# Kernel optimization log

Hardware: AMD Instinct MI355X
Metric: run time of the kernel (lower is better)

## Reference

```python
import jax, jax.numpy as jnp
import numpy as np

# dims
B, N, D = 256, 77, 768     # batch, CLIP tokens, token dim
K, Dn, H = 16, 768, 8      # nodes, node dim, heads
HID, L = 512, 2            # edge-MLP hidden, num GNN layers


def setup_inputs() -> dict:
    key = jax.random.key(0)
    ks = jax.random.split(key, 12)
    g = lambda k, shape, s=0.02: (jax.random.normal(k, shape, jnp.float32) * s)
    return {
        "w": jax.random.normal(ks[0], (B, N, D), jnp.float32),
        "token_mask": jax.random.randint(ks[1], (B, N), 0, 2).astype(jnp.int32),
        "node_queries": g(ks[2], (1, K, Dn)),
        "Wq": g(ks[3], (Dn, Dn)), "bq": jnp.zeros((Dn,), jnp.float32),
        "Wk": g(ks[4], (D, Dn)),  "bk": jnp.zeros((Dn,), jnp.float32),
        "Wv": g(ks[5], (D, Dn)),  "bv": jnp.zeros((Dn,), jnp.float32),
        "We1": g(ks[6], (2 * Dn, HID)), "be1": jnp.zeros((HID,), jnp.float32),
        "We2": g(ks[7], (HID, 1)),      "be2": jnp.zeros((1,), jnp.float32),
        "fuse_gate": jnp.float32(0.0),
        "Wg": g(ks[8], (L, Dn, Dn)), "bg": jnp.zeros((L, Dn), jnp.float32),
    }


def _edge_logits(V, We1, be1, We2, be2):
    # edge_mlp(cat[Vi, Vj]) without materializing [B,K,K,2Dn]:
    # split first linear into the Vi-half and Vj-half of its weight.
    hi = V @ We1[:Dn]   # [B,K,HID]
    hj = V @ We1[Dn:]   # [B,K,HID]
    h = jax.nn.relu(hi[:, :, None, :] + hj[:, None, :, :] + be1)  # [B,K,K,HID]
    return jnp.einsum('bijh,h->bij', h, We2[:, 0]) + be2[0]       # [B,K,K]


def _forward(w, node_queries, Wq, bq, Wk, bk, Wv, bv,
             We1, be1, We2, be2, fuse_gate, Wg, bg, token_mask):
    q = jnp.broadcast_to(node_queries, (B, K, Dn))
    Q = q @ Wq + bq        # [B,K,Dn]
    Kt = w @ Wk + bk       # [B,N,Dn]
    Vt = w @ Wv + bv       # [B,N,Dn]
    # per-head dot products summed over heads == full Dn dot product
    scale = (Dn // H) ** -0.5
    scores = jnp.einsum('bkd,bnd->bkn', Q, Kt) * scale  # [B,K,N]
    pad = (token_mask == 0)[:, None, :]                 # [B,1,N]
    scores = jnp.where(pad, jnp.finfo(scores.dtype).min, scores)
    # softmax over K per token (transpose to [B,N,K])
    S = jax.nn.softmax(jnp.swapaxes(scores, 1, 2), axis=-1)  # [B,N,K]
    V = jnp.einsum('bnk,bnd->bkd', S, Vt)                    # [B,K,Dn]
    gate = jax.nn.sigmoid(fuse_gate)
    V = (1.0 - gate) * V + gate * q
    # pre-GNN edge logits, then relational GNN refinement
    E = _edge_logits(V, We1, be1, We2, be2)
    A = jax.nn.softmax(E, axis=-1)  # [B,K,K], fixed across layers
    for l in range(L):
        msg = jnp.einsum('bij,bjd->bid', A, V @ Wg[l] + bg[l])
        V = V + jax.nn.relu(msg)
    # post-GNN edge logits
    E = _edge_logits(V, We1, be1, We2, be2)
    return S, V, E


def reference(w, token_mask, node_queries, Wq, bq, Wk, bk, Wv, bv,
              We1, be1, We2, be2, fuse_gate, Wg, bg):
    return _forward(w, node_queries, Wq, bq, Wk, bk, Wv, bv,
                    We1, be1, We2, be2, fuse_gate, Wg, bg, token_mask)
```

## Files before the change

kernel.cpp:

```cpp
#include <hip/hip_runtime.h>

typedef unsigned short u16;
typedef __attribute__((ext_vector_type(8))) short short8;
typedef __attribute__((ext_vector_type(4))) float f32x4;

#define DEV static __device__ __forceinline__

DEV float bf2f(u16 u) { return __uint_as_float(((unsigned)u) << 16); }
DEV u16 f2bf(float f) {
  unsigned u = __float_as_uint(f);
  return (u16)((u + 0x7fffu + ((u >> 16) & 1u)) >> 16);
}

DEV void cp16(void* lds, const void* g) {
  __builtin_amdgcn_global_load_lds(
      (const __attribute__((address_space(1))) unsigned int*)g,
      (__attribute__((address_space(3))) unsigned int*)lds, 16, 0, 0);
}


__global__ __launch_bounds__(256) void wcast_k(const float* __restrict__ src,
                                               u16* __restrict__ dst, int n8) {
  int i = blockIdx.x * 256 + threadIdx.x;
  if (i >= n8) return;
  f32x4 a = *(const f32x4*)&src[(size_t)i * 8];
  f32x4 b = *(const f32x4*)&src[(size_t)i * 8 + 4];
  short8 o;
#pragma unroll
  for (int e = 0; e < 4; ++e) { o[e] = (short)f2bf(a[e]); o[e + 4] = (short)f2bf(b[e]); }
  *(short8*)&dst[(size_t)i * 8] = o;
}

__global__ __launch_bounds__(256) void tcast_all(const float* __restrict__ Wv,
                                                 const float* __restrict__ We1,
                                                 const float* __restrict__ Wg,
                                                 u16* __restrict__ WvT,
                                                 u16* __restrict__ We1T,
                                                 u16* __restrict__ WgT) {
  __shared__ float tile[32][33];
  const float* src; u16* dst; int C;
  switch (blockIdx.z) {
    case 0: src = Wv;           dst = WvT;           C = 768; break;
    case 1: src = We1;          dst = We1T;          C = 512; break;
    case 2: src = We1 + 393216; dst = We1T + 393216; C = 512; break;
    case 3: src = Wg;           dst = WgT;           C = 768; break;
    default: src = Wg + 589824; dst = WgT + 589824;  C = 768; break;
  }
  int r0 = blockIdx.y * 32, c0 = blockIdx.x * 32;
  if (c0 >= C) return;
  int tr = threadIdx.x >> 5, tc = threadIdx.x & 31;
#pragma unroll
  for (int rr = 0; rr < 4; ++rr)
    tile[tr + rr * 8][tc] = src[(size_t)(r0 + tr + rr * 8) * C + c0 + tc];
  __syncthreads();
#pragma unroll
  for (int rr = 0; rr < 4; ++rr)
    dst[(size_t)(c0 + tr + rr * 8) * 768 + r0 + tc] = f2bf(tile[tc][tr + rr * 8]);
}

__global__ __launch_bounds__(256) void q_part(const float* __restrict__ nq,
                                              const float* __restrict__ Wq,
                                              float* __restrict__ Qpart) {
  int gid = blockIdx.x * 256 + threadIdx.x;
  int s = blockIdx.y;
  int k = gid / 768, d = gid % 768;
  const float* nr = nq + k * 768 + s * 96;
  const float* wp = Wq + (size_t)(s * 96) * 768 + d;
  float s0 = 0.f, s1 = 0.f, s2 = 0.f, s3 = 0.f;
#pragma unroll
  for (int c = 0; c < 96; c += 4) {
    s0 += nr[c + 0] * wp[(size_t)(c + 0) * 768];
    s1 += nr[c + 1] * wp[(size_t)(c + 1) * 768];
    s2 += nr[c + 2] * wp[(size_t)(c + 2) * 768];
    s3 += nr[c + 3] * wp[(size_t)(c + 3) * 768];
  }
  Qpart[(size_t)s * 12288 + gid] = (s0 + s1) + (s2 + s3);
}

__global__ __launch_bounds__(256) void q_reduce(const float* __restrict__ Qpart,
                                                const float* __restrict__ bq,
                                                float* __restrict__ Qf) {
  int gid = blockIdx.x * 256 + threadIdx.x;
  int d = gid % 768;
  float s = bq[d];
#pragma unroll
  for (int i = 0; i < 8; ++i) s += Qpart[(size_t)i * 12288 + gid];
  Qf[gid] = s;
}

__global__ __launch_bounds__(256) void pt_kernel(const float* __restrict__ Qf,
                                                 const float* __restrict__ Wk,
                                                 const float* __restrict__ bk,
                                                 u16* __restrict__ PT16,
                                                 float* __restrict__ qb) {
  int t = threadIdx.x;
  if (blockIdx.x == 48) {
    int k = t >> 4, j = t & 15;
    const float* q = Qf + k * 768 + j * 48;
    const float* bp = bk + j * 48;
    float s = 0.f;
#pragma unroll
    for (int d = 0; d < 48; d += 4) {
      f32x4 qv = *(const f32x4*)&q[d];
      f32x4 bv4 = *(const f32x4*)&bp[d];
      s += qv[0] * bv4[0] + qv[1] * bv4[1] + qv[2] * bv4[2] + qv[3] * bv4[3];
    }
#pragma unroll
    for (int off = 1; off < 16; off <<= 1) s += __shfl_xor(s, off);
    if (j == 0) qb[k] = s;
    return;
  }
  int gid = blockIdx.x * 256 + t;
  int c = gid >> 4, k = gid & 15;
  const float* wr = Wk + (size_t)c * 768;
  const float* q = Qf + k * 768;
  float s = 0.f;
  for (int d = 0; d < 768; d += 4) {
    f32x4 wv = *(const f32x4*)&wr[d];
    f32x4 qv = *(const f32x4*)&q[d];
    s += wv[0] * qv[0] + wv[1] * qv[1] + wv[2] * qv[2] + wv[3] * qv[3];
  }
  PT16[k * 768 + c] = f2bf(s);
}

__global__ __launch_bounds__(256) void score2(const u16* __restrict__ w16,
                                              const u16* __restrict__ PT16,
                                              const float* __restrict__ qb,
                                              const int* __restrict__ mask,
                                              float* __restrict__ Sout) {
  __shared__ u16 Ps[16 * 776];
  int t = threadIdx.x, wave = t >> 6, lane = t & 63, l16 = lane & 15, quad = lane >> 4;
  int m0 = blockIdx.x * 64;
#pragma unroll
  for (int r = 0; r < 6; ++r) {
    int idx = t + 256 * r;
    int row = idx / 96, c8 = idx % 96;
    *(short8*)&Ps[row * 776 + c8 * 8] = *(const short8*)&PT16[row * 768 + c8 * 8];
  }
  __syncthreads();
  int row = m0 + wave * 16 + l16;
  const u16* ap = w16 + (size_t)row * 768 + quad * 8;
  f32x4 acc = {0.f, 0.f, 0.f, 0.f};
#pragma unroll
  for (int it = 0; it < 24; ++it) {
    short8 fa = *(const short8*)(ap + it * 32);
    short8 fb = *(const short8*)&Ps[l16 * 776 + it * 32 + quad * 8];
    acc = __builtin_amdgcn_mfma_f32_16x16x32_bf16(fa, fb, acc, 0, 0, 0);
  }
  float qv = qb[l16];
  const float scale = 0.1020620726159658f;
#pragma unroll
  for (int r = 0; r < 4; ++r) {
    int orow = m0 + wave * 16 + quad * 4 + r;
    float s = (acc[r] + qv) * scale;
    if (mask[orow] == 0) s = -3.402823466e38f;
    float mx = s;
#pragma unroll
    for (int off = 1; off < 16; off <<= 1) mx = fmaxf(mx, __shfl_xor(mx, off));
    float e = __expf(s - mx);
    float sm = e;
#pragma unroll
    for (int off = 1; off < 16; off <<= 1) sm += __shfl_xor(sm, off);
    Sout[(size_t)orow * 16 + l16] = e / sm;
  }
}

__global__ __launch_bounds__(256) void u_kernel(const float* __restrict__ Sg,
                                                const u16* __restrict__ w16,
                                                u16* __restrict__ U16,
                                                float* __restrict__ sk) {
  __shared__ float Ss[1232];
  int b = blockIdx.x, t = threadIdx.x;
  int d = blockIdx.y * 256 + t;
#pragma unroll
  for (int r = 0; r < 5; ++r) {
    int idx = t + 256 * r;
    if (idx < 1232) Ss[idx] = Sg[(size_t)b * 1232 + idx];
  }
  __syncthreads();
  float a[16];
#pragma unroll
  for (int k = 0; k < 16; ++k) a[k] = 0.f;
  const u16* wp = w16 + (size_t)b * 59136;
  for (int n = 0; n < 77; ++n) {
    float g = bf2f(wp[(size_t)n * 768 + d]);
    const float* sr = &Ss[n * 16];
#pragma unroll
    for (int k = 0; k < 16; ++k) a[k] += sr[k] * g;
  }
#pragma unroll
  for (int k = 0; k < 16; ++k)
    U16[(size_t)b * 12288 + (size_t)k * 768 + d] = f2bf(a[k]);
  if (blockIdx.y == 0 && t < 16) {
    float s = 0.f;
    for (int n = 0; n < 77; ++n) s += Ss[n * 16 + t];
    sk[b * 16 + t] = s;
  }
}

__global__ __launch_bounds__(256) void vgemm(const u16* __restrict__ A,
                                             const u16* __restrict__ BT,
                                             const float* __restrict__ skp,
                                             const float* __restrict__ bv,
                                             const float* __restrict__ nq,
                                             const float* __restrict__ gatep,
                                             float* __restrict__ V32,
                                             u16* __restrict__ V16) {
  __shared__ u16 As[64 * 32];
  __shared__ u16 Bs[128 * 32];
  int mi = blockIdx.x / 6, ni = blockIdx.x % 6;
  int m0 = mi * 64, n0 = ni * 128;
  int t = threadIdx.x;
  int wave = t >> 6, lane = t & 63, l16 = lane & 15, quad = lane >> 4;
  int ra = wave * 16 + (lane >> 2);
  int rb1 = wave * 32 + (lane >> 2);
  int rb2 = rb1 + 16;
  int cslot = lane & 3;
  int cga = (cslot ^ ((ra >> 1) & 3)) * 8;
  int cgb1 = (cslot ^ ((rb1 >> 1) & 3)) * 8;
  int cgb2 = (cslot ^ ((rb2 >> 1) & 3)) * 8;

  f32x4 zero4 = {0.f, 0.f, 0.f, 0.f};
  f32x4 acc[4][2];
#pragma unroll
  for (int i = 0; i < 4; ++i) { acc[i][0] = zero4; acc[i][1] = zero4; }

  for (int k0 = 0; k0 < 768; k0 += 32) {
    cp16(&As[(wave * 16) * 32],      A + (size_t)(m0 + ra) * 768 + k0 + cga);
    cp16(&Bs[(wave * 32) * 32],      BT + (size_t)(n0 + rb1) * 768 + k0 + cgb1);
    cp16(&Bs[(wave * 32 + 16) * 32], BT + (size_t)(n0 + rb2) * 768 + k0 + cgb2);
    __syncthreads();
    short8 fa[4], fb[2];
#pragma unroll
    for (int i = 0; i < 4; ++i) {
      int R = i * 16 + l16;
      fa[i] = *(const short8*)&As[R * 32 + (quad ^ ((R >> 1) & 3)) * 8];
    }
#pragma unroll
    for (int j = 0; j < 2; ++j) {
      int R = wave * 32 + j * 16 + l16;
      fb[j] = *(const short8*)&Bs[R * 32 + (quad ^ ((R >> 1) & 3)) * 8];
    }
#pragma unroll
    for (int i = 0; i < 4; ++i)
#pragma unroll
      for (int j = 0; j < 2; ++j)
        acc[i][j] = __builtin_amdgcn_mfma_f32_16x16x32_bf16(fa[i], fb[j], acc[i][j], 0, 0, 0);
    __syncthreads();
  }

  float gv = gatep[0];
  float g = 1.f / (1.f + __expf(-gv)), og = 1.f - g;
  int narr[2]; float bvj[2];
#pragma unroll
  for (int j = 0; j < 2; ++j) {
    narr[j] = n0 + wave * 32 + j * 16 + l16;
    bvj[j] = bv[narr[j]];
  }
#pragma unroll
  for (int i = 0; i < 4; ++i)
#pragma unroll
    for (int r = 0; r < 4; ++r) {
      int m = m0 + i * 16 + quad * 4 + r;
      float skv = skp[m];
      size_t mrow = (size_t)m * 768;
      const float* nqr = nq + (m & 15) * 768;
#pragma unroll
      for (int j = 0; j < 2; ++j) {
        float val = acc[i][j][r] + skv * bvj[j];
        float v = og * val + g * nqr[narr[j]];
        V32[mrow + narr[j]] = v;
        V16[mrow + narr[j]] = f2bf(v);
      }
    }
}

__global__ __launch_bounds__(256) void gemm16s(const u16* __restrict__ A,
                                               const u16* __restrict__ BT0,
                                               const float* __restrict__ bias0,
                                               u16* __restrict__ C0, int N0, int ntA,
                                               const u16* __restrict__ BT1,
                                               const float* __restrict__ bias1,
                                               u16* __restrict__ C1, int N1, int ntB,
                                               int K) {
  __shared__ u16 As[64 * 32];
  __shared__ u16 Bs[128 * 32];
  int nt = ntA + ntB;
  int mi = blockIdx.x / nt, ni = blockIdx.x % nt;
  const u16* BT; const float* bias; u16* C; int N, n0;
  if (ni < ntA) { BT = BT0; bias = bias0; C = C0; N = N0; n0 = ni * 128; }
  else          { BT = BT1; bias = bias1; C = C1; N = N1; n0 = (ni - ntA) * 128; }
  int m0 = mi * 64;
  int t = threadIdx.x;
  int wave = t >> 6, lane = t & 63, l16 = lane & 15, quad = lane >> 4;
  int ra = wave * 16 + (lane >> 2);
  int rb1 = wave * 32 + (lane >> 2);
  int rb2 = rb1 + 16;
  int cslot = lane & 3;
  int cga = (cslot ^ ((ra >> 1) & 3)) * 8;
  int cgb1 = (cslot ^ ((rb1 >> 1) & 3)) * 8;
  int cgb2 = (cslot ^ ((rb2 >> 1) & 3)) * 8;

  f32x4 zero4 = {0.f, 0.f, 0.f, 0.f};
  f32x4 acc[4][2];
#pragma unroll
  for (int i = 0; i < 4; ++i) { acc[i][0] = zero4; acc[i][1] = zero4; }

  for (int k0 = 0; k0 < K; k0 += 32) {
    cp16(&As[(wave * 16) * 32],      A + (size_t)(m0 + ra) * K + k0 + cga);
    cp16(&Bs[(wave * 32) * 32],      BT + (size_t)(n0 + rb1) * K + k0 + cgb1);
    cp16(&Bs[(wave * 32 + 16) * 32], BT + (size_t)(n0 + rb2) * K + k0 + cgb2);
    __syncthreads();
    short8 fa[4], fb[2];
#pragma unroll
    for (int i = 0; i < 4; ++i) {
      int R = i * 16 + l16;
      fa[i] = *(const short8*)&As[R * 32 + (quad ^ ((R >> 1) & 3)) * 8];
    }
#pragma unroll
    for (int j = 0; j < 2; ++j) {
      int R = wave * 32 + j * 16 + l16;
      fb[j] = *(const short8*)&Bs[R * 32 + (quad ^ ((R >> 1) & 3)) * 8];
    }
#pragma unroll
    for (int i = 0; i < 4; ++i)
#pragma unroll
      for (int j = 0; j < 2; ++j)
        acc[i][j] = __builtin_amdgcn_mfma_f32_16x16x32_bf16(fa[i], fb[j], acc[i][j], 0, 0, 0);
    __syncthreads();
  }

  int narr[2]; float bvj[2];
#pragma unroll
  for (int j = 0; j < 2; ++j) {
    narr[j] = n0 + wave * 32 + j * 16 + l16;
    bvj[j] = bias ? bias[narr[j]] : 0.f;
  }
#pragma unroll
  for (int i = 0; i < 4; ++i)
#pragma unroll
    for (int r = 0; r < 4; ++r) {
      size_t mrow = (size_t)(m0 + i * 16 + quad * 4 + r) * N;
#pragma unroll
      for (int j = 0; j < 2; ++j)
        C[mrow + narr[j]] = f2bf(acc[i][j][r] + bvj[j]);
    }
}

__global__ __launch_bounds__(256) void edge_kernel(const u16* __restrict__ HIJ,
                                                   const float* __restrict__ be1,
                                                   const float* __restrict__ We2,
                                                   const float* __restrict__ be2v,
                                                   float* __restrict__ Aout,
                                                   float* __restrict__ Eout) {
  __shared__ float hiS[16 * 260];
  __shared__ float hjS[16 * 260];
  __shared__ float be1s[512];
  __shared__ float w2s[512];
  int b = blockIdx.x, t = threadIdx.x;
  be1s[t] = be1[t]; be1s[t + 256] = be1[t + 256];
  w2s[t] = We2[t];  w2s[t + 256] = We2[t + 256];

  int i = t >> 4, jj = t & 15;
  float e = 0.f;
  for (int half = 0; half < 2; ++half) {
    __syncthreads();
#pragma unroll
    for (int r = 0; r < 2; ++r) {
      int idx = t + 256 * r;
      int row = idx >> 5, c8 = idx & 31;
      const u16* src = &HIJ[(size_t)(b * 16 + row) * 1024 + half * 256 + c8 * 8];
      short8 hv = *(const short8*)src;
      short8 jv = *(const short8*)(src + 512);
      f32x4 l0, l1, m0v, m1v;
#pragma unroll
      for (int ee = 0; ee < 4; ++ee) {
        l0[ee] = bf2f((u16)hv[ee]); l1[ee] = bf2f((u16)hv[ee + 4]);
        m0v[ee] = bf2f((u16)jv[ee]); m1v[ee] = bf2f((u16)jv[ee + 4]);
      }
      *(f32x4*)&hiS[row * 260 + c8 * 8] = l0;
      *(f32x4*)&hiS[row * 260 + c8 * 8 + 4] = l1;
      *(f32x4*)&hjS[row * 260 + c8 * 8] = m0v;
      *(f32x4*)&hjS[row * 260 + c8 * 8 + 4] = m1v;
    }
    __syncthreads();
    const float* hi = &hiS[i * 260];
    const float* hj = &hjS[jj * 260];
    const float* b1 = &be1s[half * 256];
    const float* w2 = &w2s[half * 256];
#pragma unroll 2
    for (int h4 = 0; h4 < 64; ++h4) {
      f32x4 hv = *(const f32x4*)&hi[h4 * 4];
      f32x4 jv = *(const f32x4*)&hj[h4 * 4];
      f32x4 bv = *(const f32x4*)&b1[h4 * 4];
      f32x4 wv = *(const f32x4*)&w2[h4 * 4];
#pragma unroll
      for (int ee = 0; ee < 4; ++ee)
        e += fmaxf(hv[ee] + jv[ee] + bv[ee], 0.f) * wv[ee];
    }
  }
  e += be2v[0];

  if (Aout) {
    float mx = e;
#pragma unroll
    for (int off = 1; off < 16; off <<= 1) mx = fmaxf(mx, __shfl_xor(mx, off));
    float ex = __expf(e - mx);
    float sm = ex;
#pragma unroll
    for (int off = 1; off < 16; off <<= 1) sm += __shfl_xor(sm, off);
    Aout[(size_t)b * 256 + t] = ex / sm;
  }
  if (Eout) Eout[(size_t)b * 256 + t] = e;
}

__global__ __launch_bounds__(256) void combine_kernel(const float* __restrict__ Aws,
                                                      const u16* __restrict__ G,
                                                      float* __restrict__ V32,
                                                      u16* __restrict__ V16,
                                                      float* __restrict__ Vout) {
  __shared__ float Gs[16 * 772];
  __shared__ float As[256];
  int b = blockIdx.x, t = threadIdx.x;
#pragma unroll
  for (int r = 0; r < 6; ++r) {
    int idx = t + 256 * r;
    int row = idx / 96, c8 = idx % 96;
    short8 gv8 = *(const short8*)&G[(size_t)(b * 16 + row) * 768 + c8 * 8];
    f32x4 l0, l1;
#pragma unroll
    for (int ee = 0; ee < 4; ++ee) { l0[ee] = bf2f((u16)gv8[ee]); l1[ee] = bf2f((u16)gv8[ee + 4]); }
    *(f32x4*)&Gs[row * 772 + c8 * 8] = l0;
    *(f32x4*)&Gs[row * 772 + c8 * 8 + 4] = l1;
  }
  As[t] = Aws[(size_t)b * 256 + t];
  __syncthreads();
#pragma unroll
  for (int m = 0; m < 3; ++m) {
    int d = t + m * 256;
    float gv[16];
#pragma unroll
    for (int j = 0; j < 16; ++j) gv[j] = Gs[j * 772 + d];
#pragma unroll
    for (int i = 0; i < 16; ++i) {
      float msg = 0.f;
#pragma unroll
      for (int j = 0; j < 16; ++j) msg += As[i * 16 + j] * gv[j];
      size_t idx = (size_t)b * 12288 + (size_t)i * 768 + d;
      float v = V32[idx] + fmaxf(msg, 0.f);
      V32[idx] = v;
      V16[idx] = f2bf(v);
      if (Vout) Vout[idx] = v;
    }
  }
}

extern "C" void kernel_launch(void* const* d_in, const int* in_sizes, int n_in,
                              void* d_out, int out_size, void* d_ws, size_t ws_size,
                              hipStream_t stream) {
  const float* w    = (const float*)d_in[0];
  const int*   mask = (const int*)d_in[1];
  const float* nq   = (const float*)d_in[2];
  const float* Wq   = (const float*)d_in[3];
  const float* bq   = (const float*)d_in[4];
  const float* Wk   = (const float*)d_in[5];
  const float* bk   = (const float*)d_in[6];
  const float* Wv   = (const float*)d_in[7];
  const float* bv   = (const float*)d_in[8];
  const float* We1  = (const float*)d_in[9];
  const float* be1  = (const float*)d_in[10];
  const float* We2  = (const float*)d_in[11];
  const float* be2  = (const float*)d_in[12];
  const float* gate = (const float*)d_in[13];
  const float* Wg   = (const float*)d_in[14];
  const float* bg   = (const float*)d_in[15];

  float* ws    = (float*)d_ws;
  float* V32   = ws;
  float* Aws   = V32 + 3145728;
  float* Qpart = Aws + 65536;
  float* Qf    = Qpart + 98304;
  float* qb    = Qf + 12288;
  float* sk    = qb + 16;
  u16* PT16    = (u16*)(sk + 4096);
  u16* WvT     = PT16 + 12288;
  u16* We1T    = WvT + 589824;
  u16* WgT     = We1T + 786432;
  u16* V16     = WgT + 1179648;
  u16* U16     = V16 + 3145728;
  u16* w16     = U16 + 3145728;
  u16* HIJ     = w16;
  u16* Gws     = w16 + 4194304;

  float* out  = (float*)d_out;
  float* Sout = out;
  float* Vout = out + 315392;
  float* Eout = out + 315392 + 3145728;

  dim3 blk(256);

  tcast_all<<<dim3(24, 24, 5), blk, 0, stream>>>(Wv, We1, Wg, WvT, We1T, WgT);
  wcast_k<<<7392, blk, 0, stream>>>(w, w16, 1892352);
  q_part<<<dim3(48, 8), blk, 0, stream>>>(nq, Wq, Qpart);
  q_reduce<<<48, blk, 0, stream>>>(Qpart, bq, Qf);
  pt_kernel<<<49, blk, 0, stream>>>(Qf, Wk, bk, PT16, qb);

  score2<<<308, blk, 0, stream>>>(w16, PT16, qb, mask, Sout);

  u_kernel<<<dim3(256, 3), blk, 0, stream>>>(Sout, w16, U16, sk);
  vgemm<<<384, blk, 0, stream>>>(U16, WvT, sk, bv, nq, gate, V32, V16);

  gemm16s<<<896, blk, 0, stream>>>(V16, We1T, nullptr, HIJ, 1024, 8,
                                   WgT, bg, Gws, 768, 6, 768);
  edge_kernel<<<256, blk, 0, stream>>>(HIJ, be1, We2, be2, Aws, (float*)nullptr);
  combine_kernel<<<256, blk, 0, stream>>>(Aws, Gws, V32, V16, (float*)nullptr);

  gemm16s<<<384, blk, 0, stream>>>(V16, WgT + 589824, bg + 768, Gws, 768, 6,
                                   WgT + 589824, bg + 768, Gws, 768, 0, 768);
  combine_kernel<<<256, blk, 0, stream>>>(Aws, Gws, V32, V16, Vout);

  gemm16s<<<512, blk, 0, stream>>>(V16, We1T, nullptr, HIJ, 1024, 8,
                                   We1T, nullptr, HIJ, 1024, 0, 768);
  edge_kernel<<<256, blk, 0, stream>>>(HIJ, be1, We2, be2, (float*)nullptr, Eout);
}
```

Measured before the change: 344.9 us.

## Drop w bf16 cast pass and double-buffer LDS in GEMM kernels

Removes the separate wcast_k kernel that converted w to bf16. score2 now converts fp32 w inline, and u_kernel reads fp32 w directly. This saves a full write and reread of a roughly 60 MB tensor, at the cost of those kernels reading fp32, which is twice the bytes of bf16. Separately, vgemm and gemm16s now double-buffer their LDS tiles so the next k-tile's global-to-LDS copy overlaps the current MFMA work, using an explicit vmcnt drain plus barrier instead of two syncthreads per iteration.

New measurement: 330.4 us. 1.04x faster.

```diff
diff --git a/kernel.cpp b/kernel.cpp
--- a/kernel.cpp
+++ b/kernel.cpp
@@ -18,18 +18,8 @@
       (__attribute__((address_space(3))) unsigned int*)lds, 16, 0, 0);
 }
 
-
-__global__ __launch_bounds__(256) void wcast_k(const float* __restrict__ src,
-                                               u16* __restrict__ dst, int n8) {
-  int i = blockIdx.x * 256 + threadIdx.x;
-  if (i >= n8) return;
-  f32x4 a = *(const f32x4*)&src[(size_t)i * 8];
-  f32x4 b = *(const f32x4*)&src[(size_t)i * 8 + 4];
-  short8 o;
-#pragma unroll
-  for (int e = 0; e < 4; ++e) { o[e] = (short)f2bf(a[e]); o[e + 4] = (short)f2bf(b[e]); }
-  *(short8*)&dst[(size_t)i * 8] = o;
-}
+DEV void vm_drain() { asm volatile("s_waitcnt vmcnt(0)" ::: "memory"); }
+
 
 __global__ __launch_bounds__(256) void tcast_all(const float* __restrict__ Wv,
                                                  const float* __restrict__ We1,
@@ -123,7 +113,7 @@
   PT16[k * 768 + c] = f2bf(s);
 }
 
-__global__ __launch_bounds__(256) void score2(const u16* __restrict__ w16,
+__global__ __launch_bounds__(256) void score2(const float* __restrict__ w,
                                               const u16* __restrict__ PT16,
                                               const float* __restrict__ qb,
                                               const int* __restrict__ mask,
@@ -139,11 +129,15 @@
   }
   __syncthreads();
   int row = m0 + wave * 16 + l16;
-  const u16* ap = w16 + (size_t)row * 768 + quad * 8;
+  const float* ap = w + (size_t)row * 768 + quad * 8;
   f32x4 acc = {0.f, 0.f, 0.f, 0.f};
 #pragma unroll
   for (int it = 0; it < 24; ++it) {
-    short8 fa = *(const short8*)(ap + it * 32);
+    f32x4 a0 = *(const f32x4*)(ap + it * 32);
+    f32x4 a1 = *(const f32x4*)(ap + it * 32 + 4);
+    short8 fa;
+#pragma unroll
+    for (int e = 0; e < 4; ++e) { fa[e] = (short)f2bf(a0[e]); fa[e + 4] = (short)f2bf(a1[e]); }
     short8 fb = *(const short8*)&Ps[l16 * 776 + it * 32 + quad * 8];
     acc = __builtin_amdgcn_mfma_f32_16x16x32_bf16(fa, fb, acc, 0, 0, 0);
   }
@@ -166,7 +160,7 @@
 }
 
 __global__ __launch_bounds__(256) void u_kernel(const float* __restrict__ Sg,
-                                                const u16* __restrict__ w16,
+                                                const float* __restrict__ w,
                                                 u16* __restrict__ U16,
                                                 float* __restrict__ sk) {
   __shared__ float Ss[1232];
@@ -181,9 +175,9 @@
   float a[16];
 #pragma unroll
   for (int k = 0; k < 16; ++k) a[k] = 0.f;
-  const u16* wp = w16 + (size_t)b * 59136;
+  const float* wp = w + (size_t)b * 59136;
   for (int n = 0; n < 77; ++n) {
-    float g = bf2f(wp[(size_t)n * 768 + d]);
+    float g = wp[(size_t)n * 768 + d];
     const float* sr = &Ss[n * 16];
 #pragma unroll
     for (int k = 0; k < 16; ++k) a[k] += sr[k] * g;
@@ -206,8 +200,8 @@
                                              const float* __restrict__ gatep,
                                              float* __restrict__ V32,
                                              u16* __restrict__ V16) {
-  __shared__ u16 As[64 * 32];
-  __shared__ u16 Bs[128 * 32];
+  __shared__ u16 As[2 * 64 * 32];
+  __shared__ u16 Bs[2 * 128 * 32];
   int mi = blockIdx.x / 6, ni = blockIdx.x % 6;
   int m0 = mi * 64, n0 = ni * 128;
   int t = threadIdx.x;
@@ -220,33 +214,51 @@
   int cgb1 = (cslot ^ ((rb1 >> 1) & 3)) * 8;
   int cgb2 = (cslot ^ ((rb2 >> 1) & 3)) * 8;
 
+  const u16* Ap = A + (size_t)(m0 + ra) * 768 + cga;
+  const u16* Bp1 = BT + (size_t)(n0 + rb1) * 768 + cgb1;
+  const u16* Bp2 = BT + (size_t)(n0 + rb2) * 768 + cgb2;
+  u16* AsW = &As[(wave * 16) * 32];
+  u16* BsW1 = &Bs[(wave * 32) * 32];
+  u16* BsW2 = &Bs[(wave * 32 + 16) * 32];
+
   f32x4 zero4 = {0.f, 0.f, 0.f, 0.f};
   f32x4 acc[4][2];
 #pragma unroll
   for (int i = 0; i < 4; ++i) { acc[i][0] = zero4; acc[i][1] = zero4; }
 
+  cp16(AsW, Ap); cp16(BsW1, Bp1); cp16(BsW2, Bp2);
+  vm_drain();
+  __builtin_amdgcn_s_barrier();
+
+  int cur = 0;
   for (int k0 = 0; k0 < 768; k0 += 32) {
-    cp16(&As[(wave * 16) * 32],      A + (size_t)(m0 + ra) * 768 + k0 + cga);
-    cp16(&Bs[(wave * 32) * 32],      BT + (size_t)(n0 + rb1) * 768 + k0 + cgb1);
-    cp16(&Bs[(wave * 32 + 16) * 32], BT + (size_t)(n0 + rb2) * 768 + k0 + cgb2);
-    __syncthreads();
+    int nxt = cur ^ 1;
+    if (k0 + 32 < 768) {
+      cp16(AsW + nxt * 2048, Ap + k0 + 32);
+      cp16(BsW1 + nxt * 4096, Bp1 + k0 + 32);
+      cp16(BsW2 + nxt * 4096, Bp2 + k0 + 32);
+    }
+    const u16* Ab = &As[cur * 2048];
+    const u16* Bb = &Bs[cur * 4096];
     short8 fa[4], fb[2];
 #pragma unroll
     for (int i = 0; i < 4; ++i) {
       int R = i * 16 + l16;
-      fa[i] = *(const short8*)&As[R * 32 + (quad ^ ((R >> 1) & 3)) * 8];
+      fa[i] = *(const short8*)&Ab[R * 32 + (quad ^ ((R >> 1) & 3)) * 8];
     }
 #pragma unroll
     for (int j = 0; j < 2; ++j) {
       int R = wave * 32 + j * 16 + l16;
-      fb[j] = *(const short8*)&Bs[R * 32 + (quad ^ ((R >> 1) & 3)) * 8];
+      fb[j] = *(const short8*)&Bb[R * 32 + (quad ^ ((R >> 1) & 3)) * 8];
     }
 #pragma unroll
     for (int i = 0; i < 4; ++i)
 #pragma unroll
       for (int j = 0; j < 2; ++j)
         acc[i][j] = __builtin_amdgcn_mfma_f32_16x16x32_bf16(fa[i], fb[j], acc[i][j], 0, 0, 0);
-    __syncthreads();
+    vm_drain();
+    __builtin_amdgcn_s_barrier();
+    cur = nxt;
   }
 
   float gv = gatep[0];
@@ -283,8 +295,8 @@
                                                const float* __restrict__ bias1,
                                                u16* __restrict__ C1, int N1, int ntB,
                                                int K) {
-  __shared__ u16 As[64 * 32];
-  __shared__ u16 Bs[128 * 32];
+  __shared__ u16 As[2 * 64 * 32];
+  __shared__ u16 Bs[2 * 128 * 32];
   int nt = ntA + ntB;
   int mi = blockIdx.x / nt, ni = blockIdx.x % nt;
   const u16* BT; const float* bias; u16* C; int N, n0;
@@ -301,33 +313,51 @@
   int cgb1 = (cslot ^ ((rb1 >> 1) & 3)) * 8;
   int cgb2 = (cslot ^ ((rb2 >> 1) & 3)) * 8;
 
+  const u16* Ap = A + (size_t)(m0 + ra) * K + cga;
+  const u16* Bp1 = BT + (size_t)(n0 + rb1) * K + cgb1;
+  const u16* Bp2 = BT + (size_t)(n0 + rb2) * K + cgb2;
+  u16* AsW = &As[(wave * 16) * 32];
+  u16* BsW1 = &Bs[(wave * 32) * 32];
+  u16* BsW2 = &Bs[(wave * 32 + 16) * 32];
+
   f32x4 zero4 = {0.f, 0.f, 0.f, 0.f};
   f32x4 acc[4][2];
 #pragma unroll
   for (int i = 0; i < 4; ++i) { acc[i][0] = zero4; acc[i][1] = zero4; }
 
+  cp16(AsW, Ap); cp16(BsW1, Bp1); cp16(BsW2, Bp2);
+  vm_drain();
+  __builtin_amdgcn_s_barrier();
+
+  int cur = 0;
   for (int k0 = 0; k0 < K; k0 += 32) {
-    cp16(&As[(wave * 16) * 32],      A + (size_t)(m0 + ra) * K + k0 + cga);
-    cp16(&Bs[(wave * 32) * 32],      BT + (size_t)(n0 + rb1) * K + k0 + cgb1);
-    cp16(&Bs[(wave * 32 + 16) * 32], BT + (size_t)(n0 + rb2) * K + k0 + cgb2);
-    __syncthreads();
+    int nxt = cur ^ 1;
+    if (k0 + 32 < K) {
+      cp16(AsW + nxt * 2048, Ap + k0 + 32);
+      cp16(BsW1 + nxt * 4096, Bp1 + k0 + 32);
+      cp16(BsW2 + nxt * 4096, Bp2 + k0 + 32);
+    }
+    const u16* Ab = &As[cur * 2048];
+    const u16* Bb = &Bs[cur * 4096];
     short8 fa[4], fb[2];
 #pragma unroll
     for (int i = 0; i < 4; ++i) {
       int R = i * 16 + l16;
-      fa[i] = *(const short8*)&As[R * 32 + (quad ^ ((R >> 1) & 3)) * 8];
+      fa[i] = *(const short8*)&Ab[R * 32 + (quad ^ ((R >> 1) & 3)) * 8];
     }
 #pragma unroll
     for (int j = 0; j < 2; ++j) {
       int R = wave * 32 + j * 16 + l16;
-      fb[j] = *(const short8*)&Bs[R * 32 + (quad ^ ((R >> 1) & 3)) * 8];
+      fb[j] = *(const short8*)&Bb[R * 32 + (quad ^ ((R >> 1) & 3)) * 8];
     }
 #pragma unroll
     for (int i = 0; i < 4; ++i)
 #pragma unroll
       for (int j = 0; j < 2; ++j)
         acc[i][j] = __builtin_amdgcn_mfma_f32_16x16x32_bf16(fa[i], fb[j], acc[i][j], 0, 0, 0);
-    __syncthreads();
+    vm_drain();
+    __builtin_amdgcn_s_barrier();
+    cur = nxt;
   }
 
   int narr[2]; float bvj[2];
@@ -488,9 +518,8 @@
   u16* WgT     = We1T + 786432;
   u16* V16     = WgT + 1179648;
   u16* U16     = V16 + 3145728;
-  u16* w16     = U16 + 3145728;
-  u16* HIJ     = w16;
-  u16* Gws     = w16 + 4194304;
+  u16* HIJ     = U16 + 3145728;
+  u16* Gws     = HIJ + 4194304;
 
   float* out  = (float*)d_out;
   float* Sout = out;
@@ -500,14 +529,13 @@
   dim3 blk(256);
 
   tcast_all<<<dim3(24, 24, 5), blk, 0, stream>>>(Wv, We1, Wg, WvT, We1T, WgT);
-  wcast_k<<<7392, blk, 0, stream>>>(w, w16, 1892352);
   q_part<<<dim3(48, 8), blk, 0, stream>>>(nq, Wq, Qpart);
   q_reduce<<<48, blk, 0, stream>>>(Qpart, bq, Qf);
   pt_kernel<<<49, blk, 0, stream>>>(Qf, Wk, bk, PT16, qb);
 
-  score2<<<308, blk, 0, stream>>>(w16, PT16, qb, mask, Sout);
-
-  u_kernel<<<dim3(256, 3), blk, 0, stream>>>(Sout, w16, U16, sk);
+  score2<<<308, blk, 0, stream>>>(w, PT16, qb, mask, Sout);
+
+  u_kernel<<<dim3(256, 3), blk, 0, stream>>>(Sout, w, U16, sk);
   vgemm<<<384, blk, 0, stream>>>(U16, WvT, sk, bv, nq, gate, V32, V16);
 
   gemm16s<<<896, blk, 0, stream>>>(V16, We1T, nullptr, HIJ, 1024, 8,
```
